# Kernel optimization log

Hardware: AMD Instinct MI355X
Metric: run time of the kernel (lower is better)

The kernel has to match this reference:

```python
import jax, jax.numpy as jnp
import numpy as np

NEG_INF = float(np.finfo(np.float32).min)
B, KLEN, QLEN, KDIM, QDIM, ADIM, H = 2, 2048, 2048, 512, 512, 512, 8
D_K = ADIM // H


def setup_inputs() -> dict:
    key = jax.random.key(0)
    ks = jax.random.split(key, 12)
    s = 0.05  # param init scale
    inp = {
        "key_in": jax.random.normal(ks[0], (B, KLEN, KDIM), jnp.float32),
        "value_in": jax.random.normal(ks[1], (B, KLEN, KDIM), jnp.float32),
        "query_in": jax.random.normal(ks[2], (B, QLEN, QDIM), jnp.float32),
        "Wk": jax.random.normal(ks[3], (KDIM, ADIM), jnp.float32) * s,
        "bk": jax.random.normal(ks[4], (ADIM,), jnp.float32) * s,
        "Wv": jax.random.normal(ks[5], (KDIM, ADIM), jnp.float32) * s,
        "bv": jax.random.normal(ks[6], (ADIM,), jnp.float32) * s,
        "Wq": jax.random.normal(ks[7], (QDIM, ADIM), jnp.float32) * s,
        "bq": jax.random.normal(ks[8], (ADIM,), jnp.float32) * s,
        "Wo": jax.random.normal(ks[9], (ADIM, KDIM), jnp.float32) * s,
        "bo": jax.random.normal(ks[10], (KDIM,), jnp.float32) * s,
    }
    # key-length padding mask, [B, qlen, klen]; 0 = masked
    klens = jnp.array([KLEN, KLEN - 512], jnp.int32)
    valid = (jnp.arange(KLEN)[None, :] < klens[:, None]).astype(jnp.int32)  # [B, klen]
    inp["mask"] = jnp.broadcast_to(valid[:, None, :], (B, QLEN, KLEN))
    return inp


def reference(key_in, value_in, query_in, Wk, bk, Wv, bv, Wq, bq, Wo, bo, mask):
    # projections -> [B, L, H, d_k]
    k = (key_in @ Wk + bk).reshape(B, KLEN, H, D_K)
    v = (value_in @ Wv + bv).reshape(B, KLEN, H, D_K)
    q = (query_in @ Wq + bq).reshape(B, QLEN, H, D_K)
    # scaled dot-product scores [B, H, qlen, klen]
    e = jnp.einsum('bqhd,bkhd->bhqk', q, k) / jnp.sqrt(jnp.float32(D_K))
    e = jnp.where(mask[:, None, :, :] == 0, NEG_INF, e)
    aw = jax.nn.softmax(e, axis=-1)  # dropout p=0.0 -> identity
    cv = jnp.einsum('bhqk,bkhd->bqhd', aw, v).reshape(B, QLEN, ADIM)
    cv = cv @ Wo + bo  # [B, qlen, kdim]
    return cv, aw
```

## Files before the change

### kernel.cpp

```cpp
#include <hip/hip_runtime.h>

typedef short sh8 __attribute__((ext_vector_type(8)));
typedef float fx4 __attribute__((ext_vector_type(4)));

__device__ __forceinline__ unsigned short f2bf(float f) {
    union { float f; unsigned u; } v; v.f = f;
    unsigned r = v.u + 0x7FFFu + ((v.u >> 16) & 1u);
    return (unsigned short)(r >> 16);
}
__device__ __forceinline__ unsigned pk2(float a, float b) {
    return (unsigned)f2bf(a) | ((unsigned)f2bf(b) << 16);
}
__device__ __forceinline__ void gl16(const unsigned short* g, unsigned short* l) {
    __builtin_amdgcn_global_load_lds(
        (const __attribute__((address_space(1))) unsigned int*)g,
        (__attribute__((address_space(3))) unsigned int*)l, 16, 0, 0);
}

__global__ __launch_bounds__(256) void prep(const float* __restrict__ x0,
                                            const float* __restrict__ x1,
                                            const float* __restrict__ x2,
                                            const float* __restrict__ w0,
                                            const float* __restrict__ w1,
                                            const float* __restrict__ w2,
                                            const float* __restrict__ w3,
                                            const int* __restrict__ mask,
                                            unsigned short* __restrict__ in_bf,
                                            unsigned short* __restrict__ wt,
                                            unsigned long long* __restrict__ mp2) {
    __shared__ float tw[32][33];
    const int bid = blockIdx.x, tid = threadIdx.x;
    if (bid < 1536) {
        const int z = bid >> 9, xb = bid & 511;
        const float* src = z == 0 ? x0 : (z == 1 ? x1 : x2);
        unsigned short* dst = in_bf + (size_t)z * 2097152;
        for (int i = xb * 256 + tid; i < 524288; i += 131072) {
            float4 v = ((const float4*)src)[i];
            ushort4 o;
            o.x = f2bf(v.x); o.y = f2bf(v.y); o.z = f2bf(v.z); o.w = f2bf(v.w);
            ((ushort4*)dst)[i] = o;
        }
    } else if (bid < 2560) {
        const int t = bid - 1536;
        const int z = t >> 8, bx = t & 15, by = (t >> 4) & 15;
        const float* W = z == 0 ? w0 : z == 1 ? w1 : z == 2 ? w2 : w3;
        unsigned short* Wt = wt + (size_t)z * 262144;
        const int tx = tid & 31, ty = tid >> 5;
        #pragma unroll
        for (int i = 0; i < 4; ++i)
            tw[ty + i * 8][tx] = W[(size_t)(by * 32 + ty + i * 8) * 512 + bx * 32 + tx];
        __syncthreads();
        #pragma unroll
        for (int i = 0; i < 4; ++i)
            Wt[(size_t)(bx * 32 + ty + i * 8) * 512 + by * 32 + tx] = f2bf(tw[tx][ty + i * 8]);
    } else {
        const int p = bid - 2560;
        const int b = p >> 3, k = (p & 7) * 256 + tid;
        int v = mask[(size_t)b * 4194304 + k];
        unsigned long long bal = __ballot(v != 0);
        if ((tid & 63) == 0) mp2[b * 32 + (k >> 6)] = bal;
    }
}

template <int MODE>
__global__ __launch_bounds__(256) void gemm_k(const unsigned short* __restrict__ Aall,
                                              const unsigned short* __restrict__ Wtall,
                                              const float* __restrict__ b0,
                                              const float* __restrict__ b1,
                                              const float* __restrict__ b2,
                                              void* __restrict__ outp,
                                              unsigned short* __restrict__ VtB) {
    const int z = blockIdx.z;
    const unsigned short* A  = Aall  + (size_t)z * (4096 * 512);
    const unsigned short* Bt = Wtall + (size_t)z * (512 * 512);
    const float* bias = (MODE == 0) ? (z == 0 ? b0 : (z == 1 ? b1 : b2)) : b0;

    __shared__ __align__(16) unsigned short As[128 * 64];
    __shared__ __align__(16) unsigned short Bs[64 * 64];

    const int tid = threadIdx.x;
    const int wid = tid >> 6, lane = tid & 63, lr = lane & 15, lg = lane >> 4;
    const int wr = wid >> 1, wc = wid & 1;
    const int mblk = blockIdx.x * 128, nblk = blockIdx.y * 64;
    const int r7 = lr & 7;

    fx4 acc[4][2];
    #pragma unroll
    for (int mf = 0; mf < 4; ++mf)
        #pragma unroll
        for (int nf = 0; nf < 2; ++nf)
            #pragma unroll
            for (int j = 0; j < 4; ++j) acc[mf][nf][j] = 0.f;

    for (int kt = 0; kt < 8; ++kt) {
        __syncthreads();
        #pragma unroll
        for (int g = 0; g < 4; ++g) {
            int ci = wid * 256 + g * 64 + lane;
            int r = ci >> 3, c = (ci & 7) ^ (r & 7);
            gl16(A + (size_t)(mblk + r) * 512 + kt * 64 + c * 8, &As[(wid * 256 + g * 64) * 8]);
        }
        #pragma unroll
        for (int g = 0; g < 2; ++g) {
            int ci = wid * 128 + g * 64 + lane;
            int r = ci >> 3, c = (ci & 7) ^ (r & 7);
            gl16(Bt + (size_t)(nblk + r) * 512 + kt * 64 + c * 8, &Bs[(wid * 128 + g * 64) * 8]);
        }
        __syncthreads();
        #pragma unroll
        for (int d = 0; d < 2; ++d) {
            sh8 af[4], bf[2];
            #pragma unroll
            for (int mf = 0; mf < 4; ++mf)
                af[mf] = *(const sh8*)&As[(wr * 64 + mf * 16 + lr) * 64 + (((d * 4 + lg) ^ r7) * 8)];
            #pragma unroll
            for (int nf = 0; nf < 2; ++nf)
                bf[nf] = *(const sh8*)&Bs[(wc * 32 + nf * 16 + lr) * 64 + (((d * 4 + lg) ^ r7) * 8)];
            #pragma unroll
            for (int mf = 0; mf < 4; ++mf)
                #pragma unroll
                for (int nf = 0; nf < 2; ++nf)
                    acc[mf][nf] = __builtin_amdgcn_mfma_f32_16x16x32_bf16(af[mf], bf[nf], acc[mf][nf], 0, 0, 0);
        }
    }

    if (MODE == 0 && z == 1) {
        #pragma unroll
        for (int nf = 0; nf < 2; ++nf) {
            int n = nblk + wc * 32 + nf * 16 + lr;
            float bv = bias[n];
            int h = n >> 6, dd = n & 63;
            #pragma unroll
            for (int mf = 0; mf < 4; ++mf) {
                int m0 = mblk + wr * 64 + mf * 16 + lg * 4;
                int bb = m0 >> 11, lq = m0 & 2047;
                ushort4 o;
                o.x = f2bf(acc[mf][nf][0] + bv);
                o.y = f2bf(acc[mf][nf][1] + bv);
                o.z = f2bf(acc[mf][nf][2] + bv);
                o.w = f2bf(acc[mf][nf][3] + bv);
                *(ushort4*)(VtB + ((size_t)(bb * 8 + h) * 64 + dd) * 2048 + lq) = o;
            }
        }
    } else {
        #pragma unroll
        for (int nf = 0; nf < 2; ++nf) {
            int n = nblk + wc * 32 + nf * 16 + lr;
            float bv = bias[n];
            #pragma unroll
            for (int mf = 0; mf < 4; ++mf) {
                #pragma unroll
                for (int j = 0; j < 4; ++j) {
                    int m = mblk + wr * 64 + mf * 16 + lg * 4 + j;
                    float val = acc[mf][nf][j] + bv;
                    if (MODE == 0) {
                        if (z == 2) val *= 0.125f;
                        int bb = m >> 11, lq = m & 2047, h = n >> 6, dd = n & 63;
                        ((unsigned short*)outp)[(size_t)(((z * 2 + bb) * 8 + h) * 2048 + lq) * 64 + dd] = f2bf(val);
                    } else {
                        ((float*)outp)[(size_t)m * 512 + n] = val;
                    }
                }
            }
        }
    }
}

__device__ __forceinline__ void stage_k1(const unsigned short* Kg, unsigned short* sK,
                                         int t, int w, int lane) {
    #pragma unroll
    for (int g = 0; g < 2; ++g) {
        int ci = w * 128 + g * 64 + lane;
        int r = ci >> 3, c = (ci & 7) ^ (r & 7);
        gl16(Kg + (size_t)(t * 64 + r) * 64 + c * 8, sK + (w * 128 + g * 64) * 8);
    }
}
__device__ __forceinline__ void stage_kv(const unsigned short* Kg, const unsigned short* Vg,
                                         unsigned short* sK, unsigned short* sV,
                                         int t, int w, int lane) {
    #pragma unroll
    for (int g = 0; g < 2; ++g) {
        int ci = w * 128 + g * 64 + lane;
        int r = ci >> 3, c = (ci & 7) ^ (r & 7);
        gl16(Kg + (size_t)(t * 64 + r) * 64 + c * 8, sK + (w * 128 + g * 64) * 8);
        gl16(Vg + (size_t)r * 2048 + t * 64 + c * 8, sV + (w * 128 + g * 64) * 8);
    }
}

__global__ __launch_bounds__(256, 2) void attn_fused(const unsigned short* __restrict__ qkv,
                                                     const unsigned short* __restrict__ Vt,
                                                     const unsigned long long* __restrict__ mp2,
                                                     float* __restrict__ aw,
                                                     unsigned short* __restrict__ cv) {
    const int bid = blockIdx.x;
    const int swz = (bid & 7) * 64 + (bid >> 3);
    const int qb = swz & 31, bh = swz >> 5;
    const int b = bh >> 3, h = bh & 7;
    const unsigned short* Kg = qkv + (size_t)bh * 131072;
    const unsigned short* Vg = Vt + (size_t)bh * 131072;
    const unsigned short* Qg = qkv + 2 * 2097152 + (size_t)bh * 131072 + (size_t)qb * 4096;

    __shared__ __align__(16) unsigned short Ks[2][4096];
    __shared__ __align__(16) unsigned short Vs[2][4096];
    __shared__ __align__(16) unsigned short Pb[4096];

    const int tid = threadIdx.x, w = tid >> 6, lane = tid & 63, lr = lane & 15, lg = lane >> 4;
    const int r7 = lr & 7;
    const int q = qb * 64 + w * 16 + lr;

    sh8 qf0 = *(const sh8*)(Qg + (w * 16 + lr) * 64 + lg * 8);
    sh8 qf1 = *(const sh8*)(Qg + (w * 16 + lr) * 64 + 32 + lg * 8);
    unsigned long long mwv = (lane < 32) ? mp2[b * 32 + lane] : 0ull;

    float m_ = -3e38f, l_ = 0.f;
    asm volatile("s_waitcnt vmcnt(0)" ::: "memory");
    stage_k1(Kg, Ks[0], 0, w, lane);
    stage_k1(Kg, Ks[1], 1, w, lane);
    for (int kt = 0; kt < 32; ++kt) {
        if (kt >= 1 && kt <= 30)
            stage_k1(Kg, Ks[(kt + 1) & 1], kt + 1, w, lane);
        if (kt == 31) asm volatile("s_waitcnt vmcnt(0)" ::: "memory");
        else          asm volatile("s_waitcnt vmcnt(2)" ::: "memory");
        asm volatile("s_barrier" ::: "memory");
        unsigned long long mw = __shfl(mwv, kt, 64);
        if (mw != 0ull) {
            const unsigned short* KsB = Ks[kt & 1];
            fx4 accs[4];
            #pragma unroll
            for (int mt = 0; mt < 4; ++mt) {
                sh8 kf0 = *(const sh8*)&KsB[(mt * 16 + lr) * 64 + ((lg ^ r7) * 8)];
                sh8 kf1 = *(const sh8*)&KsB[(mt * 16 + lr) * 64 + (((4 + lg) ^ r7) * 8)];
                fx4 zz; zz[0] = 0.f; zz[1] = 0.f; zz[2] = 0.f; zz[3] = 0.f;
                zz = __builtin_amdgcn_mfma_f32_16x16x32_bf16(kf0, qf0, zz, 0, 0, 0);
                accs[mt] = __builtin_amdgcn_mfma_f32_16x16x32_bf16(kf1, qf1, zz, 0, 0, 0);
            }
            float sv[16], tmax = -3e38f;
            if (mw == ~0ull) {
                #pragma unroll
                for (int mt = 0; mt < 4; ++mt)
                    #pragma unroll
                    for (int j = 0; j < 4; ++j) {
                        float s = accs[mt][j];
                        sv[mt * 4 + j] = s; tmax = fmaxf(tmax, s);
                    }
            } else {
                #pragma unroll
                for (int mt = 0; mt < 4; ++mt)
                    #pragma unroll
                    for (int j = 0; j < 4; ++j) {
                        int kl = mt * 16 + lg * 4 + j;
                        bool ok = (mw >> kl) & 1ull;
                        float s = ok ? accs[mt][j] : -3e38f;
                        sv[mt * 4 + j] = s; tmax = fmaxf(tmax, s);
                    }
            }
            float mnew = fmaxf(m_, tmax);
            float ps = 0.f;
            #pragma unroll
            for (int i = 0; i < 16; ++i) ps += __expf(sv[i] - mnew);
            l_ = l_ * __expf(m_ - mnew) + ps;
            m_ = mnew;
        }
        asm volatile("s_barrier" ::: "memory");
    }
    #pragma unroll
    for (int off = 16; off <= 32; off <<= 1) {
        float mo = __shfl_xor(m_, off), lo = __shfl_xor(l_, off);
        float mn = fmaxf(m_, mo);
        l_ = l_ * __expf(m_ - mn) + lo * __expf(mo - mn);
        m_ = mn;
    }
    const float M = (l_ > 0.f) ? m_ : 0.f;
    const float rinv = (l_ > 0.f) ? 1.f / l_ : 0.f;

    fx4 acco[4];
    #pragma unroll
    for (int md = 0; md < 4; ++md) { acco[md][0] = 0.f; acco[md][1] = 0.f; acco[md][2] = 0.f; acco[md][3] = 0.f; }
    float* awb = aw + (size_t)bh * 4194304 + (size_t)q * 2048;

    asm volatile("s_waitcnt vmcnt(0)" ::: "memory");
    stage_kv(Kg, Vg, Ks[0], Vs[0], 0, w, lane);
    stage_kv(Kg, Vg, Ks[1], Vs[1], 1, w, lane);

    for (int kt = 0; kt < 32; ++kt) {
        if (kt >= 1 && kt <= 30)
            stage_kv(Kg, Vg, Ks[(kt + 1) & 1], Vs[(kt + 1) & 1], kt + 1, w, lane);
        if (kt == 0 || kt == 31) asm volatile("s_waitcnt vmcnt(4)" ::: "memory");
        else                     asm volatile("s_waitcnt vmcnt(8)" ::: "memory");
        asm volatile("s_barrier" ::: "memory");

        unsigned long long mw = __shfl(mwv, kt, 64);
        const unsigned short* KsB = Ks[kt & 1];
        const unsigned short* VsB = Vs[kt & 1];

        if (mw != 0ull) {
            fx4 accs[4];
            #pragma unroll
            for (int mt = 0; mt < 4; ++mt) {
                sh8 kf0 = *(const sh8*)&KsB[(mt * 16 + lr) * 64 + ((lg ^ r7) * 8)];
                sh8 kf1 = *(const sh8*)&KsB[(mt * 16 + lr) * 64 + (((4 + lg) ^ r7) * 8)];
                fx4 zz; zz[0] = 0.f; zz[1] = 0.f; zz[2] = 0.f; zz[3] = 0.f;
                zz = __builtin_amdgcn_mfma_f32_16x16x32_bf16(kf0, qf0, zz, 0, 0, 0);
                accs[mt] = __builtin_amdgcn_mfma_f32_16x16x32_bf16(kf1, qf1, zz, 0, 0, 0);
            }
            bool full = (mw == ~0ull);
            #pragma unroll
            for (int mt = 0; mt < 4; ++mt) {
                float4 pw;
                #pragma unroll
                for (int j = 0; j < 4; ++j) {
                    int kl = mt * 16 + lg * 4 + j;
                    bool ok = full || ((mw >> kl) & 1ull);
                    float p = ok ? __expf(accs[mt][j] - M) * rinv : 0.f;
                    ((float*)&pw)[j] = p;
                }
                *(float4*)(awb + kt * 64 + mt * 16 + lg * 4) = pw;
                int sc = (mt * 2 + (lg >> 1)) ^ r7;
                *(uint2*)&Pb[(w * 16 + lr) * 64 + sc * 8 + (lg & 1) * 4] =
                    make_uint2(pk2(pw.x, pw.y), pk2(pw.z, pw.w));
            }
            asm volatile("s_waitcnt lgkmcnt(0)" ::: "memory");
            __builtin_amdgcn_sched_barrier(0);
            sh8 bp0 = *(const sh8*)&Pb[(w * 16 + lr) * 64 + ((lg ^ r7) * 8)];
            sh8 bp1 = *(const sh8*)&Pb[(w * 16 + lr) * 64 + (((4 + lg) ^ r7) * 8)];
            #pragma unroll
            for (int md = 0; md < 4; ++md) {
                sh8 vf0 = *(const sh8*)&VsB[(md * 16 + lr) * 64 + ((lg ^ r7) * 8)];
                sh8 vf1 = *(const sh8*)&VsB[(md * 16 + lr) * 64 + (((4 + lg) ^ r7) * 8)];
                acco[md] = __builtin_amdgcn_mfma_f32_16x16x32_bf16(vf0, bp0, acco[md], 0, 0, 0);
                acco[md] = __builtin_amdgcn_mfma_f32_16x16x32_bf16(vf1, bp1, acco[md], 0, 0, 0);
            }
        } else {
            float4 z4 = {0.f, 0.f, 0.f, 0.f};
            #pragma unroll
            for (int mt = 0; mt < 4; ++mt)
                *(float4*)(awb + kt * 64 + mt * 16 + lg * 4) = z4;
        }
        asm volatile("s_barrier" ::: "memory");
    }

    #pragma unroll
    for (int md = 0; md < 4; ++md) {
        ushort4 o;
        o.x = f2bf(acco[md][0]); o.y = f2bf(acco[md][1]);
        o.z = f2bf(acco[md][2]); o.w = f2bf(acco[md][3]);
        *(ushort4*)(cv + (size_t)(b * 2048 + q) * 512 + h * 64 + md * 16 + lg * 4) = o;
    }
}

extern "C" void kernel_launch(void* const* d_in, const int* in_sizes, int n_in,
                              void* d_out, int out_size, void* d_ws, size_t ws_size,
                              hipStream_t stream) {
    const float* key_in   = (const float*)d_in[0];
    const float* value_in = (const float*)d_in[1];
    const float* query_in = (const float*)d_in[2];
    const float* Wk = (const float*)d_in[3];
    const float* bk = (const float*)d_in[4];
    const float* Wv = (const float*)d_in[5];
    const float* bv = (const float*)d_in[6];
    const float* Wq = (const float*)d_in[7];
    const float* bq = (const float*)d_in[8];
    const float* Wo = (const float*)d_in[9];
    const float* bo = (const float*)d_in[10];
    const int* mask = (const int*)d_in[11];

    char* ws = (char*)d_ws;
    unsigned short* in_bf = (unsigned short*)(ws);
    unsigned short* qkv   = (unsigned short*)(ws + 12582912);
    unsigned short* cvb   = (unsigned short*)(ws + 12582912 + 4194304);
    unsigned short* wt    = (unsigned short*)(ws + 25165824);
    unsigned short* VtB   = (unsigned short*)(ws + 27262976);
    unsigned long long* mp2 = (unsigned long long*)(ws + 31457280);

    float* out_cv = (float*)d_out;
    float* out_aw = (float*)d_out + 2097152;

    prep<<<dim3(2576), 256, 0, stream>>>(key_in, value_in, query_in,
                                         Wk, Wv, Wq, Wo, mask, in_bf, wt, mp2);
    gemm_k<0><<<dim3(32, 8, 3), 256, 0, stream>>>(in_bf, wt, bk, bv, bq, qkv, VtB);
    attn_fused<<<dim3(512), 256, 0, stream>>>(qkv, VtB, mp2, out_aw, cvb);
    gemm_k<1><<<dim3(32, 8, 1), 256, 0, stream>>>(cvb, wt + 3 * 262144, bo, bo, bo, out_cv, (unsigned short*)nullptr);
}
```

Before: 126.5 us.

## Split key tiles across waves with direct global K/V loads and LDS reduction

Changes the attention kernel so each wave owns a quarter of the key tiles for all 64 queries, instead of owning 16 queries over all keys. K and V fragments are read straight from global memory rather than staged through double-buffered LDS, which removes the per-tile barriers. Per-wave softmax statistics and partial PV accumulators are combined through shared memory at the end. Stores of the attention weights and output are made nontemporal. The trade-offs are more registers (16 accumulators, Q fragments for 4 groups), possible load imbalance between waves because of the mask, and a serialized four-pass LDS reduction.

```diff
diff --git a/kernel.cpp b/kernel.cpp
--- a/kernel.cpp
+++ b/kernel.cpp
@@ -2,6 +2,8 @@
 
 typedef short sh8 __attribute__((ext_vector_type(8)));
 typedef float fx4 __attribute__((ext_vector_type(4)));
+typedef float fl4 __attribute__((ext_vector_type(4)));
+typedef unsigned short us4 __attribute__((ext_vector_type(4)));
 
 __device__ __forceinline__ unsigned short f2bf(float f) {
     union { float f; unsigned u; } v; v.f = f;
@@ -166,27 +168,6 @@
     }
 }
 
-__device__ __forceinline__ void stage_k1(const unsigned short* Kg, unsigned short* sK,
-                                         int t, int w, int lane) {
-    #pragma unroll
-    for (int g = 0; g < 2; ++g) {
-        int ci = w * 128 + g * 64 + lane;
-        int r = ci >> 3, c = (ci & 7) ^ (r & 7);
-        gl16(Kg + (size_t)(t * 64 + r) * 64 + c * 8, sK + (w * 128 + g * 64) * 8);
-    }
-}
-__device__ __forceinline__ void stage_kv(const unsigned short* Kg, const unsigned short* Vg,
-                                         unsigned short* sK, unsigned short* sV,
-                                         int t, int w, int lane) {
-    #pragma unroll
-    for (int g = 0; g < 2; ++g) {
-        int ci = w * 128 + g * 64 + lane;
-        int r = ci >> 3, c = (ci & 7) ^ (r & 7);
-        gl16(Kg + (size_t)(t * 64 + r) * 64 + c * 8, sK + (w * 128 + g * 64) * 8);
-        gl16(Vg + (size_t)r * 2048 + t * 64 + c * 8, sV + (w * 128 + g * 64) * 8);
-    }
-}
-
 __global__ __launch_bounds__(256, 2) void attn_fused(const unsigned short* __restrict__ qkv,
                                                      const unsigned short* __restrict__ Vt,
                                                      const unsigned long long* __restrict__ mp2,
@@ -200,151 +181,195 @@
     const unsigned short* Vg = Vt + (size_t)bh * 131072;
     const unsigned short* Qg = qkv + 2 * 2097152 + (size_t)bh * 131072 + (size_t)qb * 4096;
 
-    __shared__ __align__(16) unsigned short Ks[2][4096];
-    __shared__ __align__(16) unsigned short Vs[2][4096];
-    __shared__ __align__(16) unsigned short Pb[4096];
+    __shared__ __align__(16) unsigned short Pb[4][4096];
+    __shared__ float2 sm[4][64];
+    __shared__ __align__(16) float pvr[64][68];
 
     const int tid = threadIdx.x, w = tid >> 6, lane = tid & 63, lr = lane & 15, lg = lane >> 4;
     const int r7 = lr & 7;
-    const int q = qb * 64 + w * 16 + lr;
-
-    sh8 qf0 = *(const sh8*)(Qg + (w * 16 + lr) * 64 + lg * 8);
-    sh8 qf1 = *(const sh8*)(Qg + (w * 16 + lr) * 64 + 32 + lg * 8);
-    unsigned long long mwv = (lane < 32) ? mp2[b * 32 + lane] : 0ull;
-
-    float m_ = -3e38f, l_ = 0.f;
-    asm volatile("s_waitcnt vmcnt(0)" ::: "memory");
-    stage_k1(Kg, Ks[0], 0, w, lane);
-    stage_k1(Kg, Ks[1], 1, w, lane);
-    for (int kt = 0; kt < 32; ++kt) {
-        if (kt >= 1 && kt <= 30)
-            stage_k1(Kg, Ks[(kt + 1) & 1], kt + 1, w, lane);
-        if (kt == 31) asm volatile("s_waitcnt vmcnt(0)" ::: "memory");
-        else          asm volatile("s_waitcnt vmcnt(2)" ::: "memory");
-        asm volatile("s_barrier" ::: "memory");
-        unsigned long long mw = __shfl(mwv, kt, 64);
-        if (mw != 0ull) {
-            const unsigned short* KsB = Ks[kt & 1];
-            fx4 accs[4];
+
+    sh8 qf[4][2];
+    #pragma unroll
+    for (int qg = 0; qg < 4; ++qg) {
+        qf[qg][0] = *(const sh8*)(Qg + (qg * 16 + lr) * 64 + lg * 8);
+        qf[qg][1] = *(const sh8*)(Qg + (qg * 16 + lr) * 64 + 32 + lg * 8);
+    }
+
+    float m_[4], l_[4];
+    #pragma unroll
+    for (int qg = 0; qg < 4; ++qg) { m_[qg] = -3e38f; l_[qg] = 0.f; }
+
+    for (int t = 0; t < 8; ++t) {
+        unsigned long long mw = mp2[b * 32 + w * 8 + t];
+        if (mw == 0ull) continue;
+        const unsigned short* Kt = Kg + (size_t)(w * 8 + t) * 4096;
+        sh8 kf0[4], kf1[4];
+        #pragma unroll
+        for (int mt = 0; mt < 4; ++mt) {
+            kf0[mt] = *(const sh8*)(Kt + (mt * 16 + lr) * 64 + lg * 8);
+            kf1[mt] = *(const sh8*)(Kt + (mt * 16 + lr) * 64 + 32 + lg * 8);
+        }
+        bool full = (mw == ~0ull);
+        #pragma unroll
+        for (int qg = 0; qg < 4; ++qg) {
+            fx4 a[4];
             #pragma unroll
             for (int mt = 0; mt < 4; ++mt) {
-                sh8 kf0 = *(const sh8*)&KsB[(mt * 16 + lr) * 64 + ((lg ^ r7) * 8)];
-                sh8 kf1 = *(const sh8*)&KsB[(mt * 16 + lr) * 64 + (((4 + lg) ^ r7) * 8)];
                 fx4 zz; zz[0] = 0.f; zz[1] = 0.f; zz[2] = 0.f; zz[3] = 0.f;
-                zz = __builtin_amdgcn_mfma_f32_16x16x32_bf16(kf0, qf0, zz, 0, 0, 0);
-                accs[mt] = __builtin_amdgcn_mfma_f32_16x16x32_bf16(kf1, qf1, zz, 0, 0, 0);
+                zz = __builtin_amdgcn_mfma_f32_16x16x32_bf16(kf0[mt], qf[qg][0], zz, 0, 0, 0);
+                a[mt] = __builtin_amdgcn_mfma_f32_16x16x32_bf16(kf1[mt], qf[qg][1], zz, 0, 0, 0);
             }
             float sv[16], tmax = -3e38f;
-            if (mw == ~0ull) {
-                #pragma unroll
-                for (int mt = 0; mt < 4; ++mt)
-                    #pragma unroll
-                    for (int j = 0; j < 4; ++j) {
-                        float s = accs[mt][j];
-                        sv[mt * 4 + j] = s; tmax = fmaxf(tmax, s);
-                    }
-            } else {
-                #pragma unroll
-                for (int mt = 0; mt < 4; ++mt)
-                    #pragma unroll
-                    for (int j = 0; j < 4; ++j) {
-                        int kl = mt * 16 + lg * 4 + j;
-                        bool ok = (mw >> kl) & 1ull;
-                        float s = ok ? accs[mt][j] : -3e38f;
-                        sv[mt * 4 + j] = s; tmax = fmaxf(tmax, s);
-                    }
-            }
-            float mnew = fmaxf(m_, tmax);
-            float ps = 0.f;
-            #pragma unroll
-            for (int i = 0; i < 16; ++i) ps += __expf(sv[i] - mnew);
-            l_ = l_ * __expf(m_ - mnew) + ps;
-            m_ = mnew;
-        }
-        asm volatile("s_barrier" ::: "memory");
-    }
-    #pragma unroll
-    for (int off = 16; off <= 32; off <<= 1) {
-        float mo = __shfl_xor(m_, off), lo = __shfl_xor(l_, off);
-        float mn = fmaxf(m_, mo);
-        l_ = l_ * __expf(m_ - mn) + lo * __expf(mo - mn);
-        m_ = mn;
-    }
-    const float M = (l_ > 0.f) ? m_ : 0.f;
-    const float rinv = (l_ > 0.f) ? 1.f / l_ : 0.f;
-
-    fx4 acco[4];
-    #pragma unroll
-    for (int md = 0; md < 4; ++md) { acco[md][0] = 0.f; acco[md][1] = 0.f; acco[md][2] = 0.f; acco[md][3] = 0.f; }
-    float* awb = aw + (size_t)bh * 4194304 + (size_t)q * 2048;
-
-    asm volatile("s_waitcnt vmcnt(0)" ::: "memory");
-    stage_kv(Kg, Vg, Ks[0], Vs[0], 0, w, lane);
-    stage_kv(Kg, Vg, Ks[1], Vs[1], 1, w, lane);
-
-    for (int kt = 0; kt < 32; ++kt) {
-        if (kt >= 1 && kt <= 30)
-            stage_kv(Kg, Vg, Ks[(kt + 1) & 1], Vs[(kt + 1) & 1], kt + 1, w, lane);
-        if (kt == 0 || kt == 31) asm volatile("s_waitcnt vmcnt(4)" ::: "memory");
-        else                     asm volatile("s_waitcnt vmcnt(8)" ::: "memory");
-        asm volatile("s_barrier" ::: "memory");
-
-        unsigned long long mw = __shfl(mwv, kt, 64);
-        const unsigned short* KsB = Ks[kt & 1];
-        const unsigned short* VsB = Vs[kt & 1];
-
-        if (mw != 0ull) {
-            fx4 accs[4];
-            #pragma unroll
-            for (int mt = 0; mt < 4; ++mt) {
-                sh8 kf0 = *(const sh8*)&KsB[(mt * 16 + lr) * 64 + ((lg ^ r7) * 8)];
-                sh8 kf1 = *(const sh8*)&KsB[(mt * 16 + lr) * 64 + (((4 + lg) ^ r7) * 8)];
-                fx4 zz; zz[0] = 0.f; zz[1] = 0.f; zz[2] = 0.f; zz[3] = 0.f;
-                zz = __builtin_amdgcn_mfma_f32_16x16x32_bf16(kf0, qf0, zz, 0, 0, 0);
-                accs[mt] = __builtin_amdgcn_mfma_f32_16x16x32_bf16(kf1, qf1, zz, 0, 0, 0);
-            }
-            bool full = (mw == ~0ull);
-            #pragma unroll
-            for (int mt = 0; mt < 4; ++mt) {
-                float4 pw;
+            #pragma unroll
+            for (int mt = 0; mt < 4; ++mt)
                 #pragma unroll
                 for (int j = 0; j < 4; ++j) {
                     int kl = mt * 16 + lg * 4 + j;
                     bool ok = full || ((mw >> kl) & 1ull);
-                    float p = ok ? __expf(accs[mt][j] - M) * rinv : 0.f;
-                    ((float*)&pw)[j] = p;
+                    float s = ok ? a[mt][j] : -3e38f;
+                    sv[mt * 4 + j] = s; tmax = fmaxf(tmax, s);
                 }
-                *(float4*)(awb + kt * 64 + mt * 16 + lg * 4) = pw;
+            float mnew = fmaxf(m_[qg], tmax);
+            if (mnew > -1e37f) {
+                float ps = 0.f;
+                #pragma unroll
+                for (int i = 0; i < 16; ++i) ps += __expf(sv[i] - mnew);
+                l_[qg] = l_[qg] * __expf(m_[qg] - mnew) + ps;
+                m_[qg] = mnew;
+            }
+        }
+    }
+    #pragma unroll
+    for (int qg = 0; qg < 4; ++qg) {
+        #pragma unroll
+        for (int off = 16; off <= 32; off <<= 1) {
+            float mo = __shfl_xor(m_[qg], off), lo = __shfl_xor(l_[qg], off);
+            float mn = fmaxf(m_[qg], mo);
+            l_[qg] = l_[qg] * __expf(m_[qg] - mn) + lo * __expf(mo - mn);
+            m_[qg] = mn;
+        }
+        if (lg == 0) sm[w][qg * 16 + lr] = make_float2(m_[qg], l_[qg]);
+    }
+    __syncthreads();
+    float M[4], R[4];
+    #pragma unroll
+    for (int qg = 0; qg < 4; ++qg) {
+        float mm = -3e38f;
+        float2 pv4[4];
+        #pragma unroll
+        for (int u = 0; u < 4; ++u) { pv4[u] = sm[u][qg * 16 + lr]; mm = fmaxf(mm, pv4[u].x); }
+        float ll = 0.f;
+        #pragma unroll
+        for (int u = 0; u < 4; ++u) ll += pv4[u].y * __expf(pv4[u].x - mm);
+        M[qg] = (ll > 0.f) ? mm : 0.f;
+        R[qg] = (ll > 0.f) ? 1.f / ll : 0.f;
+    }
+
+    fx4 acco[4][4];
+    #pragma unroll
+    for (int md = 0; md < 4; ++md)
+        #pragma unroll
+        for (int qg = 0; qg < 4; ++qg) { acco[md][qg][0]=0.f; acco[md][qg][1]=0.f; acco[md][qg][2]=0.f; acco[md][qg][3]=0.f; }
+
+    float* awb = aw + (size_t)bh * 4194304 + (size_t)(qb * 64) * 2048;
+    unsigned short* PbW = Pb[w];
+
+    for (int t = 0; t < 8; ++t) {
+        const int ktg = w * 8 + t;
+        unsigned long long mw = mp2[b * 32 + ktg];
+        if (mw == 0ull) {
+            fl4 z4 = {0.f, 0.f, 0.f, 0.f};
+            #pragma unroll
+            for (int qg = 0; qg < 4; ++qg)
+                #pragma unroll
+                for (int mt = 0; mt < 4; ++mt)
+                    __builtin_nontemporal_store(z4,
+                        (fl4*)(awb + (size_t)(qg * 16 + lr) * 2048 + ktg * 64 + mt * 16 + lg * 4));
+            continue;
+        }
+        const unsigned short* Kt = Kg + (size_t)ktg * 4096;
+        sh8 kf0[4], kf1[4];
+        #pragma unroll
+        for (int mt = 0; mt < 4; ++mt) {
+            kf0[mt] = *(const sh8*)(Kt + (mt * 16 + lr) * 64 + lg * 8);
+            kf1[mt] = *(const sh8*)(Kt + (mt * 16 + lr) * 64 + 32 + lg * 8);
+        }
+        bool full = (mw == ~0ull);
+        #pragma unroll
+        for (int qg = 0; qg < 4; ++qg) {
+            fx4 a[4];
+            #pragma unroll
+            for (int mt = 0; mt < 4; ++mt) {
+                fx4 zz; zz[0] = 0.f; zz[1] = 0.f; zz[2] = 0.f; zz[3] = 0.f;
+                zz = __builtin_amdgcn_mfma_f32_16x16x32_bf16(kf0[mt], qf[qg][0], zz, 0, 0, 0);
+                a[mt] = __builtin_amdgcn_mfma_f32_16x16x32_bf16(kf1[mt], qf[qg][1], zz, 0, 0, 0);
+            }
+            #pragma unroll
+            for (int mt = 0; mt < 4; ++mt) {
+                fl4 pw;
+                #pragma unroll
+                for (int j = 0; j < 4; ++j) {
+                    int kl = mt * 16 + lg * 4 + j;
+                    bool ok = full || ((mw >> kl) & 1ull);
+                    float p = ok ? __expf(a[mt][j] - M[qg]) * R[qg] : 0.f;
+                    pw[j] = p;
+                }
+                __builtin_nontemporal_store(pw,
+                    (fl4*)(awb + (size_t)(qg * 16 + lr) * 2048 + ktg * 64 + mt * 16 + lg * 4));
                 int sc = (mt * 2 + (lg >> 1)) ^ r7;
-                *(uint2*)&Pb[(w * 16 + lr) * 64 + sc * 8 + (lg & 1) * 4] =
-                    make_uint2(pk2(pw.x, pw.y), pk2(pw.z, pw.w));
-            }
-            asm volatile("s_waitcnt lgkmcnt(0)" ::: "memory");
-            __builtin_amdgcn_sched_barrier(0);
-            sh8 bp0 = *(const sh8*)&Pb[(w * 16 + lr) * 64 + ((lg ^ r7) * 8)];
-            sh8 bp1 = *(const sh8*)&Pb[(w * 16 + lr) * 64 + (((4 + lg) ^ r7) * 8)];
-            #pragma unroll
-            for (int md = 0; md < 4; ++md) {
-                sh8 vf0 = *(const sh8*)&VsB[(md * 16 + lr) * 64 + ((lg ^ r7) * 8)];
-                sh8 vf1 = *(const sh8*)&VsB[(md * 16 + lr) * 64 + (((4 + lg) ^ r7) * 8)];
-                acco[md] = __builtin_amdgcn_mfma_f32_16x16x32_bf16(vf0, bp0, acco[md], 0, 0, 0);
-                acco[md] = __builtin_amdgcn_mfma_f32_16x16x32_bf16(vf1, bp1, acco[md], 0, 0, 0);
-            }
-        } else {
-            float4 z4 = {0.f, 0.f, 0.f, 0.f};
-            #pragma unroll
-            for (int mt = 0; mt < 4; ++mt)
-                *(float4*)(awb + kt * 64 + mt * 16 + lg * 4) = z4;
-        }
-        asm volatile("s_barrier" ::: "memory");
-    }
-
-    #pragma unroll
-    for (int md = 0; md < 4; ++md) {
-        ushort4 o;
-        o.x = f2bf(acco[md][0]); o.y = f2bf(acco[md][1]);
-        o.z = f2bf(acco[md][2]); o.w = f2bf(acco[md][3]);
-        *(ushort4*)(cv + (size_t)(b * 2048 + q) * 512 + h * 64 + md * 16 + lg * 4) = o;
+                *(uint2*)&PbW[(qg * 16 + lr) * 64 + sc * 8 + (lg & 1) * 4] =
+                    make_uint2(pk2(pw[0], pw[1]), pk2(pw[2], pw[3]));
+            }
+        }
+        asm volatile("s_waitcnt lgkmcnt(0)" ::: "memory");
+        __builtin_amdgcn_sched_barrier(0);
+        sh8 pf[4][2];
+        #pragma unroll
+        for (int qg = 0; qg < 4; ++qg) {
+            pf[qg][0] = *(const sh8*)&PbW[(qg * 16 + lr) * 64 + ((lg ^ r7) * 8)];
+            pf[qg][1] = *(const sh8*)&PbW[(qg * 16 + lr) * 64 + (((4 + lg) ^ r7) * 8)];
+        }
+        __builtin_amdgcn_s_setprio(1);
+        #pragma unroll
+        for (int md = 0; md < 4; ++md) {
+            sh8 vf0 = *(const sh8*)(Vg + (size_t)(md * 16 + lr) * 2048 + ktg * 64 + lg * 8);
+            sh8 vf1 = *(const sh8*)(Vg + (size_t)(md * 16 + lr) * 2048 + ktg * 64 + 32 + lg * 8);
+            #pragma unroll
+            for (int qg = 0; qg < 4; ++qg) {
+                acco[md][qg] = __builtin_amdgcn_mfma_f32_16x16x32_bf16(vf0, pf[qg][0], acco[md][qg], 0, 0, 0);
+                acco[md][qg] = __builtin_amdgcn_mfma_f32_16x16x32_bf16(vf1, pf[qg][1], acco[md][qg], 0, 0, 0);
+            }
+        }
+        __builtin_amdgcn_s_setprio(0);
+    }
+
+    #pragma unroll
+    for (int pass = 0; pass < 4; ++pass) {
+        if (w == pass) {
+            #pragma unroll
+            for (int md = 0; md < 4; ++md)
+                #pragma unroll
+                for (int qg = 0; qg < 4; ++qg) {
+                    float* p = &pvr[qg * 16 + lr][md * 16 + lg * 4];
+                    if (pass == 0) {
+                        *(fx4*)p = acco[md][qg];
+                    } else {
+                        fx4 c = *(fx4*)p;
+                        c[0] += acco[md][qg][0]; c[1] += acco[md][qg][1];
+                        c[2] += acco[md][qg][2]; c[3] += acco[md][qg][3];
+                        *(fx4*)p = c;
+                    }
+                }
+        }
+        __syncthreads();
+    }
+    #pragma unroll
+    for (int qg = 0; qg < 4; ++qg) {
+        fx4 c = *(fx4*)&pvr[qg * 16 + lr][w * 16 + lg * 4];
+        us4 o;
+        o[0] = f2bf(c[0]); o[1] = f2bf(c[1]); o[2] = f2bf(c[2]); o[3] = f2bf(c[3]);
+        __builtin_nontemporal_store(o,
+            (us4*)(cv + (size_t)(b * 2048 + qb * 64 + qg * 16 + lr) * 512 + h * 64 + w * 16 + lg * 4));
     }
 }
 
```

Result: slower. 142.7 us (+12.8%).

## Fuse fp32-to-bf16 input conversion into QKV GEMM and use nontemporal stores

Applied to the files above, without the earlier changes.

Removes the separate conversion pass over the key/value/query inputs in prep. The QKV GEMM now loads fp32 directly, converts to bf16 in registers and writes swizzled LDS tiles. This avoids a full write and re-read of the bf16 input copies. In exchange it gives up the async global_load_lds path for the A operand, and each A tile is now read as fp32 by 8 column blocks. Attention-weight and context outputs also switch to nontemporal stores to cut cache pollution from the large write stream.

```diff
diff --git a/kernel.cpp b/kernel.cpp
--- a/kernel.cpp
+++ b/kernel.cpp
@@ -2,6 +2,8 @@
 
 typedef short sh8 __attribute__((ext_vector_type(8)));
 typedef float fx4 __attribute__((ext_vector_type(4)));
+typedef float fl4 __attribute__((ext_vector_type(4)));
+typedef unsigned short us4 __attribute__((ext_vector_type(4)));
 
 __device__ __forceinline__ unsigned short f2bf(float f) {
     union { float f; unsigned u; } v; v.f = f;
@@ -17,31 +19,17 @@
         (__attribute__((address_space(3))) unsigned int*)l, 16, 0, 0);
 }
 
-__global__ __launch_bounds__(256) void prep(const float* __restrict__ x0,
-                                            const float* __restrict__ x1,
-                                            const float* __restrict__ x2,
-                                            const float* __restrict__ w0,
+__global__ __launch_bounds__(256) void prep(const float* __restrict__ w0,
                                             const float* __restrict__ w1,
                                             const float* __restrict__ w2,
                                             const float* __restrict__ w3,
                                             const int* __restrict__ mask,
-                                            unsigned short* __restrict__ in_bf,
                                             unsigned short* __restrict__ wt,
                                             unsigned long long* __restrict__ mp2) {
     __shared__ float tw[32][33];
     const int bid = blockIdx.x, tid = threadIdx.x;
-    if (bid < 1536) {
-        const int z = bid >> 9, xb = bid & 511;
-        const float* src = z == 0 ? x0 : (z == 1 ? x1 : x2);
-        unsigned short* dst = in_bf + (size_t)z * 2097152;
-        for (int i = xb * 256 + tid; i < 524288; i += 131072) {
-            float4 v = ((const float4*)src)[i];
-            ushort4 o;
-            o.x = f2bf(v.x); o.y = f2bf(v.y); o.z = f2bf(v.z); o.w = f2bf(v.w);
-            ((ushort4*)dst)[i] = o;
-        }
-    } else if (bid < 2560) {
-        const int t = bid - 1536;
+    if (bid < 1024) {
+        const int t = bid;
         const int z = t >> 8, bx = t & 15, by = (t >> 4) & 15;
         const float* W = z == 0 ? w0 : z == 1 ? w1 : z == 2 ? w2 : w3;
         unsigned short* Wt = wt + (size_t)z * 262144;
@@ -54,7 +42,7 @@
         for (int i = 0; i < 4; ++i)
             Wt[(size_t)(bx * 32 + ty + i * 8) * 512 + by * 32 + tx] = f2bf(tw[tx][ty + i * 8]);
     } else {
-        const int p = bid - 2560;
+        const int p = bid - 1024;
         const int b = p >> 3, k = (p & 7) * 256 + tid;
         int v = mask[(size_t)b * 4194304 + k];
         unsigned long long bal = __ballot(v != 0);
@@ -63,7 +51,10 @@
 }
 
 template <int MODE>
-__global__ __launch_bounds__(256) void gemm_k(const unsigned short* __restrict__ Aall,
+__global__ __launch_bounds__(256) void gemm_k(const unsigned short* __restrict__ Abf,
+                                              const float* __restrict__ xk,
+                                              const float* __restrict__ xv,
+                                              const float* __restrict__ xq,
                                               const unsigned short* __restrict__ Wtall,
                                               const float* __restrict__ b0,
                                               const float* __restrict__ b1,
@@ -71,7 +62,7 @@
                                               void* __restrict__ outp,
                                               unsigned short* __restrict__ VtB) {
     const int z = blockIdx.z;
-    const unsigned short* A  = Aall  + (size_t)z * (4096 * 512);
+    const float* Afp = (MODE == 0) ? (z == 0 ? xk : (z == 1 ? xv : xq)) : nullptr;
     const unsigned short* Bt = Wtall + (size_t)z * (512 * 512);
     const float* bias = (MODE == 0) ? (z == 0 ? b0 : (z == 1 ? b1 : b2)) : b0;
 
@@ -94,11 +85,28 @@
 
     for (int kt = 0; kt < 8; ++kt) {
         __syncthreads();
-        #pragma unroll
-        for (int g = 0; g < 4; ++g) {
-            int ci = wid * 256 + g * 64 + lane;
-            int r = ci >> 3, c = (ci & 7) ^ (r & 7);
-            gl16(A + (size_t)(mblk + r) * 512 + kt * 64 + c * 8, &As[(wid * 256 + g * 64) * 8]);
+        if (MODE == 0) {
+            #pragma unroll
+            for (int g = 0; g < 4; ++g) {
+                int ci = g * 256 + tid;
+                int r = ci >> 3, c = ci & 7;
+                const float* src = Afp + (size_t)(mblk + r) * 512 + kt * 64 + c * 8;
+                float4 v0 = *(const float4*)(src);
+                float4 v1 = *(const float4*)(src + 4);
+                union { unsigned short u[8]; sh8 v; } pk;
+                pk.u[0] = f2bf(v0.x); pk.u[1] = f2bf(v0.y);
+                pk.u[2] = f2bf(v0.z); pk.u[3] = f2bf(v0.w);
+                pk.u[4] = f2bf(v1.x); pk.u[5] = f2bf(v1.y);
+                pk.u[6] = f2bf(v1.z); pk.u[7] = f2bf(v1.w);
+                *(sh8*)&As[r * 64 + ((c ^ (r & 7)) * 8)] = pk.v;
+            }
+        } else {
+            #pragma unroll
+            for (int g = 0; g < 4; ++g) {
+                int ci = wid * 256 + g * 64 + lane;
+                int r = ci >> 3, c = (ci & 7) ^ (r & 7);
+                gl16(Abf + (size_t)(mblk + r) * 512 + kt * 64 + c * 8, &As[(wid * 256 + g * 64) * 8]);
+            }
         }
         #pragma unroll
         for (int g = 0; g < 2; ++g) {
@@ -306,18 +314,18 @@
             bool full = (mw == ~0ull);
             #pragma unroll
             for (int mt = 0; mt < 4; ++mt) {
-                float4 pw;
+                fl4 pw;
                 #pragma unroll
                 for (int j = 0; j < 4; ++j) {
                     int kl = mt * 16 + lg * 4 + j;
                     bool ok = full || ((mw >> kl) & 1ull);
                     float p = ok ? __expf(accs[mt][j] - M) * rinv : 0.f;
-                    ((float*)&pw)[j] = p;
+                    pw[j] = p;
                 }
-                *(float4*)(awb + kt * 64 + mt * 16 + lg * 4) = pw;
+                __builtin_nontemporal_store(pw, (fl4*)(awb + kt * 64 + mt * 16 + lg * 4));
                 int sc = (mt * 2 + (lg >> 1)) ^ r7;
                 *(uint2*)&Pb[(w * 16 + lr) * 64 + sc * 8 + (lg & 1) * 4] =
-                    make_uint2(pk2(pw.x, pw.y), pk2(pw.z, pw.w));
+                    make_uint2(pk2(pw[0], pw[1]), pk2(pw[2], pw[3]));
             }
             asm volatile("s_waitcnt lgkmcnt(0)" ::: "memory");
             __builtin_amdgcn_sched_barrier(0);
@@ -331,20 +339,21 @@
                 acco[md] = __builtin_amdgcn_mfma_f32_16x16x32_bf16(vf1, bp1, acco[md], 0, 0, 0);
             }
         } else {
-            float4 z4 = {0.f, 0.f, 0.f, 0.f};
+            fl4 z4 = {0.f, 0.f, 0.f, 0.f};
             #pragma unroll
             for (int mt = 0; mt < 4; ++mt)
-                *(float4*)(awb + kt * 64 + mt * 16 + lg * 4) = z4;
+                __builtin_nontemporal_store(z4, (fl4*)(awb + kt * 64 + mt * 16 + lg * 4));
         }
         asm volatile("s_barrier" ::: "memory");
     }
 
     #pragma unroll
     for (int md = 0; md < 4; ++md) {
-        ushort4 o;
-        o.x = f2bf(acco[md][0]); o.y = f2bf(acco[md][1]);
-        o.z = f2bf(acco[md][2]); o.w = f2bf(acco[md][3]);
-        *(ushort4*)(cv + (size_t)(b * 2048 + q) * 512 + h * 64 + md * 16 + lg * 4) = o;
+        us4 o;
+        o[0] = f2bf(acco[md][0]); o[1] = f2bf(acco[md][1]);
+        o[2] = f2bf(acco[md][2]); o[3] = f2bf(acco[md][3]);
+        __builtin_nontemporal_store(o,
+            (us4*)(cv + (size_t)(b * 2048 + q) * 512 + h * 64 + md * 16 + lg * 4));
     }
 }
 
@@ -365,19 +374,19 @@
     const int* mask = (const int*)d_in[11];
 
     char* ws = (char*)d_ws;
-    unsigned short* in_bf = (unsigned short*)(ws);
-    unsigned short* qkv   = (unsigned short*)(ws + 12582912);
-    unsigned short* cvb   = (unsigned short*)(ws + 12582912 + 4194304);
-    unsigned short* wt    = (unsigned short*)(ws + 25165824);
-    unsigned short* VtB   = (unsigned short*)(ws + 27262976);
-    unsigned long long* mp2 = (unsigned long long*)(ws + 31457280);
+    unsigned short* qkv   = (unsigned short*)(ws);
+    unsigned short* cvb   = (unsigned short*)(ws + 4194304);
+    unsigned short* wt    = (unsigned short*)(ws + 12582912);
+    unsigned short* VtB   = (unsigned short*)(ws + 14680064);
+    unsigned long long* mp2 = (unsigned long long*)(ws + 18874368);
 
     float* out_cv = (float*)d_out;
     float* out_aw = (float*)d_out + 2097152;
 
-    prep<<<dim3(2576), 256, 0, stream>>>(key_in, value_in, query_in,
-                                         Wk, Wv, Wq, Wo, mask, in_bf, wt, mp2);
-    gemm_k<0><<<dim3(32, 8, 3), 256, 0, stream>>>(in_bf, wt, bk, bv, bq, qkv, VtB);
+    prep<<<dim3(1040), 256, 0, stream>>>(Wk, Wv, Wq, Wo, mask, wt, mp2);
+    gemm_k<0><<<dim3(32, 8, 3), 256, 0, stream>>>(nullptr, key_in, value_in, query_in,
+                                                  wt, bk, bv, bq, qkv, VtB);
     attn_fused<<<dim3(512), 256, 0, stream>>>(qkv, VtB, mp2, out_aw, cvb);
-    gemm_k<1><<<dim3(32, 8, 1), 256, 0, stream>>>(cvb, wt + 3 * 262144, bo, bo, bo, out_cv, (unsigned short*)nullptr);
-}
+    gemm_k<1><<<dim3(32, 8, 1), 256, 0, stream>>>(cvb, nullptr, nullptr, nullptr,
+                                                  wt + 3 * 262144, bo, bo, bo, out_cv, (unsigned short*)nullptr);
+}
```

After: 146.4 us. 1.16x slower.

## Split attention key range across two wave groups per block and merge softmax stats

Applied to the files above, without the earlier changes.

Doubles the attention block to 512 threads, with two groups of four waves each processing half of the key length (1024 keys) for the same 64 queries. Partial max/sum statistics and partial PV accumulators are merged through shared memory, and a single group writes the bf16 context. The aw and cv stores are also switched to nontemporal stores. This halves the serial loop length per block to expose more parallelism on the 512-block grid, at the cost of extra syncthreads, LDS traffic for the reductions, and higher per-block LDS and register pressure.

```diff
diff --git a/kernel.cpp b/kernel.cpp
--- a/kernel.cpp
+++ b/kernel.cpp
@@ -2,6 +2,8 @@
 
 typedef short sh8 __attribute__((ext_vector_type(8)));
 typedef float fx4 __attribute__((ext_vector_type(4)));
+typedef float fl4 __attribute__((ext_vector_type(4)));
+typedef unsigned short us4 __attribute__((ext_vector_type(4)));
 
 __device__ __forceinline__ unsigned short f2bf(float f) {
     union { float f; unsigned u; } v; v.f = f;
@@ -166,28 +168,28 @@
     }
 }
 
-__device__ __forceinline__ void stage_k1(const unsigned short* Kg, unsigned short* sK,
-                                         int t, int w, int lane) {
+__device__ __forceinline__ void stg_k(const unsigned short* Kgg, unsigned short* sK,
+                                      int t, int wq, int lane) {
     #pragma unroll
-    for (int g = 0; g < 2; ++g) {
-        int ci = w * 128 + g * 64 + lane;
+    for (int g2 = 0; g2 < 2; ++g2) {
+        int ci = wq * 128 + g2 * 64 + lane;
         int r = ci >> 3, c = (ci & 7) ^ (r & 7);
-        gl16(Kg + (size_t)(t * 64 + r) * 64 + c * 8, sK + (w * 128 + g * 64) * 8);
-    }
-}
-__device__ __forceinline__ void stage_kv(const unsigned short* Kg, const unsigned short* Vg,
-                                         unsigned short* sK, unsigned short* sV,
-                                         int t, int w, int lane) {
+        gl16(Kgg + (size_t)(t * 64 + r) * 64 + c * 8, sK + (wq * 128 + g2 * 64) * 8);
+    }
+}
+__device__ __forceinline__ void stg_kv(const unsigned short* Kgg, const unsigned short* Vg,
+                                       unsigned short* sK, unsigned short* sV,
+                                       int t, int gofs, int wq, int lane) {
     #pragma unroll
-    for (int g = 0; g < 2; ++g) {
-        int ci = w * 128 + g * 64 + lane;
+    for (int g2 = 0; g2 < 2; ++g2) {
+        int ci = wq * 128 + g2 * 64 + lane;
         int r = ci >> 3, c = (ci & 7) ^ (r & 7);
-        gl16(Kg + (size_t)(t * 64 + r) * 64 + c * 8, sK + (w * 128 + g * 64) * 8);
-        gl16(Vg + (size_t)r * 2048 + t * 64 + c * 8, sV + (w * 128 + g * 64) * 8);
-    }
-}
-
-__global__ __launch_bounds__(256, 2) void attn_fused(const unsigned short* __restrict__ qkv,
+        gl16(Kgg + (size_t)(t * 64 + r) * 64 + c * 8, sK + (wq * 128 + g2 * 64) * 8);
+        gl16(Vg + (size_t)r * 2048 + gofs + t * 64 + c * 8, sV + (wq * 128 + g2 * 64) * 8);
+    }
+}
+
+__global__ __launch_bounds__(512, 4) void attn_fused(const unsigned short* __restrict__ qkv,
                                                      const unsigned short* __restrict__ Vt,
                                                      const unsigned long long* __restrict__ mp2,
                                                      float* __restrict__ aw,
@@ -200,31 +202,37 @@
     const unsigned short* Vg = Vt + (size_t)bh * 131072;
     const unsigned short* Qg = qkv + 2 * 2097152 + (size_t)bh * 131072 + (size_t)qb * 4096;
 
-    __shared__ __align__(16) unsigned short Ks[2][4096];
-    __shared__ __align__(16) unsigned short Vs[2][4096];
-    __shared__ __align__(16) unsigned short Pb[4096];
-
-    const int tid = threadIdx.x, w = tid >> 6, lane = tid & 63, lr = lane & 15, lg = lane >> 4;
+    __shared__ __align__(16) unsigned short LB[40960];
+
+    const int tid = threadIdx.x;
+    const int w = tid >> 6, g = w >> 2, wq = w & 3;
+    const int lane = tid & 63, lr = lane & 15, lg = lane >> 4;
     const int r7 = lr & 7;
-    const int q = qb * 64 + w * 16 + lr;
-
-    sh8 qf0 = *(const sh8*)(Qg + (w * 16 + lr) * 64 + lg * 8);
-    sh8 qf1 = *(const sh8*)(Qg + (w * 16 + lr) * 64 + 32 + lg * 8);
-    unsigned long long mwv = (lane < 32) ? mp2[b * 32 + lane] : 0ull;
+    const int q = qb * 64 + wq * 16 + lr;
+    const int gofs = g * 1024;
+
+    const unsigned short* Kgg = Kg + (size_t)gofs * 64;
+    unsigned short* KsB0 = LB + g * 8192;
+    unsigned short* VsB0 = LB + 16384 + g * 8192;
+    unsigned short* PbW  = LB + 32768 + g * 4096;
+
+    sh8 qf0 = *(const sh8*)(Qg + (wq * 16 + lr) * 64 + lg * 8);
+    sh8 qf1 = *(const sh8*)(Qg + (wq * 16 + lr) * 64 + 32 + lg * 8);
+    unsigned long long mwv = (lane < 16) ? mp2[b * 32 + g * 16 + lane] : 0ull;
 
     float m_ = -3e38f, l_ = 0.f;
     asm volatile("s_waitcnt vmcnt(0)" ::: "memory");
-    stage_k1(Kg, Ks[0], 0, w, lane);
-    stage_k1(Kg, Ks[1], 1, w, lane);
-    for (int kt = 0; kt < 32; ++kt) {
-        if (kt >= 1 && kt <= 30)
-            stage_k1(Kg, Ks[(kt + 1) & 1], kt + 1, w, lane);
-        if (kt == 31) asm volatile("s_waitcnt vmcnt(0)" ::: "memory");
-        else          asm volatile("s_waitcnt vmcnt(2)" ::: "memory");
+    stg_k(Kgg, KsB0, 0, wq, lane);
+    stg_k(Kgg, KsB0 + 4096, 1, wq, lane);
+    for (int t = 0; t < 16; ++t) {
+        if (t >= 1 && t <= 14)
+            stg_k(Kgg, KsB0 + ((t + 1) & 1) * 4096, t + 1, wq, lane);
+        if (t == 15) asm volatile("s_waitcnt vmcnt(0)" ::: "memory");
+        else         asm volatile("s_waitcnt vmcnt(2)" ::: "memory");
         asm volatile("s_barrier" ::: "memory");
-        unsigned long long mw = __shfl(mwv, kt, 64);
+        unsigned long long mw = __shfl(mwv, t, 64);
         if (mw != 0ull) {
-            const unsigned short* KsB = Ks[kt & 1];
+            const unsigned short* KsB = KsB0 + (t & 1) * 4096;
             fx4 accs[4];
             #pragma unroll
             for (int mt = 0; mt < 4; ++mt) {
@@ -270,28 +278,37 @@
         l_ = l_ * __expf(m_ - mn) + lo * __expf(mo - mn);
         m_ = mn;
     }
-    const float M = (l_ > 0.f) ? m_ : 0.f;
-    const float rinv = (l_ > 0.f) ? 1.f / l_ : 0.f;
+    float2* sm = (float2*)(LB + 16384);
+    if (lg == 0) sm[g * 64 + wq * 16 + lr] = make_float2(m_, l_);
+    __syncthreads();
+    float2 s0 = sm[wq * 16 + lr];
+    float2 s1 = sm[64 + wq * 16 + lr];
+    float mm = fmaxf(s0.x, s1.x);
+    float ll = s0.y * __expf(s0.x - mm) + s1.y * __expf(s1.x - mm);
+    const float M = (ll > 0.f) ? mm : 0.f;
+    const float rinv = (ll > 0.f) ? 1.f / ll : 0.f;
+    __syncthreads();
 
     fx4 acco[4];
     #pragma unroll
     for (int md = 0; md < 4; ++md) { acco[md][0] = 0.f; acco[md][1] = 0.f; acco[md][2] = 0.f; acco[md][3] = 0.f; }
-    float* awb = aw + (size_t)bh * 4194304 + (size_t)q * 2048;
-
-    asm volatile("s_waitcnt vmcnt(0)" ::: "memory");
-    stage_kv(Kg, Vg, Ks[0], Vs[0], 0, w, lane);
-    stage_kv(Kg, Vg, Ks[1], Vs[1], 1, w, lane);
-
-    for (int kt = 0; kt < 32; ++kt) {
-        if (kt >= 1 && kt <= 30)
-            stage_kv(Kg, Vg, Ks[(kt + 1) & 1], Vs[(kt + 1) & 1], kt + 1, w, lane);
-        if (kt == 0 || kt == 31) asm volatile("s_waitcnt vmcnt(4)" ::: "memory");
-        else                     asm volatile("s_waitcnt vmcnt(8)" ::: "memory");
+    float* awb = aw + (size_t)bh * 4194304 + (size_t)q * 2048 + gofs;
+
+    stg_kv(Kgg, Vg, KsB0, VsB0, 0, gofs, wq, lane);
+    stg_kv(Kgg, Vg, KsB0 + 4096, VsB0 + 4096, 1, gofs, wq, lane);
+
+    for (int t = 0; t < 16; ++t) {
+        if (t >= 1 && t <= 14)
+            stg_kv(Kgg, Vg, KsB0 + ((t + 1) & 1) * 4096, VsB0 + ((t + 1) & 1) * 4096,
+                   t + 1, gofs, wq, lane);
+        if (t == 0)       asm volatile("s_waitcnt vmcnt(4)" ::: "memory");
+        else if (t == 15) asm volatile("s_waitcnt vmcnt(0)" ::: "memory");
+        else              asm volatile("s_waitcnt vmcnt(8)" ::: "memory");
         asm volatile("s_barrier" ::: "memory");
 
-        unsigned long long mw = __shfl(mwv, kt, 64);
-        const unsigned short* KsB = Ks[kt & 1];
-        const unsigned short* VsB = Vs[kt & 1];
+        unsigned long long mw = __shfl(mwv, t, 64);
+        const unsigned short* KsB = KsB0 + (t & 1) * 4096;
+        const unsigned short* VsB = VsB0 + (t & 1) * 4096;
 
         if (mw != 0ull) {
             fx4 accs[4];
@@ -306,23 +323,23 @@
             bool full = (mw == ~0ull);
             #pragma unroll
             for (int mt = 0; mt < 4; ++mt) {
-                float4 pw;
+                fl4 pw;
                 #pragma unroll
                 for (int j = 0; j < 4; ++j) {
                     int kl = mt * 16 + lg * 4 + j;
                     bool ok = full || ((mw >> kl) & 1ull);
                     float p = ok ? __expf(accs[mt][j] - M) * rinv : 0.f;
-                    ((float*)&pw)[j] = p;
+                    pw[j] = p;
                 }
-                *(float4*)(awb + kt * 64 + mt * 16 + lg * 4) = pw;
+                __builtin_nontemporal_store(pw, (fl4*)(awb + t * 64 + mt * 16 + lg * 4));
                 int sc = (mt * 2 + (lg >> 1)) ^ r7;
-                *(uint2*)&Pb[(w * 16 + lr) * 64 + sc * 8 + (lg & 1) * 4] =
-                    make_uint2(pk2(pw.x, pw.y), pk2(pw.z, pw.w));
+                *(uint2*)&PbW[(wq * 16 + lr) * 64 + sc * 8 + (lg & 1) * 4] =
+                    make_uint2(pk2(pw[0], pw[1]), pk2(pw[2], pw[3]));
             }
             asm volatile("s_waitcnt lgkmcnt(0)" ::: "memory");
             __builtin_amdgcn_sched_barrier(0);
-            sh8 bp0 = *(const sh8*)&Pb[(w * 16 + lr) * 64 + ((lg ^ r7) * 8)];
-            sh8 bp1 = *(const sh8*)&Pb[(w * 16 + lr) * 64 + (((4 + lg) ^ r7) * 8)];
+            sh8 bp0 = *(const sh8*)&PbW[(wq * 16 + lr) * 64 + ((lg ^ r7) * 8)];
+            sh8 bp1 = *(const sh8*)&PbW[(wq * 16 + lr) * 64 + (((4 + lg) ^ r7) * 8)];
             #pragma unroll
             for (int md = 0; md < 4; ++md) {
                 sh8 vf0 = *(const sh8*)&VsB[(md * 16 + lr) * 64 + ((lg ^ r7) * 8)];
@@ -331,20 +348,32 @@
                 acco[md] = __builtin_amdgcn_mfma_f32_16x16x32_bf16(vf1, bp1, acco[md], 0, 0, 0);
             }
         } else {
-            float4 z4 = {0.f, 0.f, 0.f, 0.f};
+            fl4 z4 = {0.f, 0.f, 0.f, 0.f};
             #pragma unroll
             for (int mt = 0; mt < 4; ++mt)
-                *(float4*)(awb + kt * 64 + mt * 16 + lg * 4) = z4;
+                __builtin_nontemporal_store(z4, (fl4*)(awb + t * 64 + mt * 16 + lg * 4));
         }
         asm volatile("s_barrier" ::: "memory");
     }
 
-    #pragma unroll
-    for (int md = 0; md < 4; ++md) {
-        ushort4 o;
-        o.x = f2bf(acco[md][0]); o.y = f2bf(acco[md][1]);
-        o.z = f2bf(acco[md][2]); o.w = f2bf(acco[md][3]);
-        *(ushort4*)(cv + (size_t)(b * 2048 + q) * 512 + h * 64 + md * 16 + lg * 4) = o;
+    float* pvr = (float*)LB;
+    if (g == 1) {
+        #pragma unroll
+        for (int md = 0; md < 4; ++md)
+            *(fx4*)&pvr[(wq * 16 + lr) * 68 + md * 16 + lg * 4] = acco[md];
+    }
+    __syncthreads();
+    if (g == 0) {
+        #pragma unroll
+        for (int md = 0; md < 4; ++md) {
+            fx4 c = *(fx4*)&pvr[(wq * 16 + lr) * 68 + md * 16 + lg * 4];
+            c[0] += acco[md][0]; c[1] += acco[md][1];
+            c[2] += acco[md][2]; c[3] += acco[md][3];
+            us4 o;
+            o[0] = f2bf(c[0]); o[1] = f2bf(c[1]); o[2] = f2bf(c[2]); o[3] = f2bf(c[3]);
+            __builtin_nontemporal_store(o,
+                (us4*)(cv + (size_t)(b * 2048 + q) * 512 + h * 64 + md * 16 + lg * 4));
+        }
     }
 }
 
@@ -378,6 +407,6 @@
     prep<<<dim3(2576), 256, 0, stream>>>(key_in, value_in, query_in,
                                          Wk, Wv, Wq, Wo, mask, in_bf, wt, mp2);
     gemm_k<0><<<dim3(32, 8, 3), 256, 0, stream>>>(in_bf, wt, bk, bv, bq, qkv, VtB);
-    attn_fused<<<dim3(512), 256, 0, stream>>>(qkv, VtB, mp2, out_aw, cvb);
+    attn_fused<<<dim3(512), 512, 0, stream>>>(qkv, VtB, mp2, out_aw, cvb);
     gemm_k<1><<<dim3(32, 8, 1), 256, 0, stream>>>(cvb, wt + 3 * 262144, bo, bo, bo, out_cv, (unsigned short*)nullptr);
 }
```

Result: slower. 149.0 us (+17.8%).
